# Optimization experiments

Hardware: AMD Instinct MI355X
Metric: run time of the kernel (lower is better)

The kernel has to match this reference:

```python
import jax, jax.numpy as jnp
import numpy as np

N, D, E, L, NL = 100000, 64, 400000, 4, 10000
NEG = jnp.float32(-1e30)


def _make_graph(key):
    k1, k2, k3, k4 = jax.random.split(key, 4)
    ncov = N - NL
    # nodes [0, NL) never appear as source -> exactly NL leaves
    src_cov = jnp.arange(ncov, dtype=jnp.int32) + NL
    src_rand = jax.random.randint(k1, (E - ncov,), NL, N, dtype=jnp.int32)
    src = jnp.concatenate([src_cov, src_rand])
    dst = jax.random.randint(k2, (E,), 0, N, dtype=jnp.int32)
    edge_index = jnp.stack([src, dst])  # [2, E]
    edge_attr = jax.random.normal(k3, (E, D), jnp.float32)
    # partition edges into L 'topological level' masks
    edge_masks = (jnp.arange(E) % L)[None, :] == jnp.arange(L)[:, None]  # [L, E] bool
    x = jax.random.normal(k4, (N, D), jnp.float32)
    return x, edge_index, edge_attr, edge_masks


def setup_inputs() -> dict:
    key = jax.random.key(0)
    kg1, kg2, kp = jax.random.split(key, 3)
    x1, ei1, ea1, em1 = _make_graph(kg1)
    x2, ei2, ea2, em2 = _make_graph(kg2)
    ks = jax.random.split(kp, 10)
    s = 1.0 / np.sqrt(D)
    params = {
        'We': jax.random.normal(ks[0], (D, D), jnp.float32) * s,
        'be': jax.random.normal(ks[1], (D,), jnp.float32) * s,
        'Wa': jax.random.normal(ks[2], (1, 2 * D), jnp.float32) * s,
        'ba': jax.random.normal(ks[3], (1,), jnp.float32) * s,
        'Wih': jax.random.normal(ks[4], (3 * D, D), jnp.float32) * s,
        'Whh': jax.random.normal(ks[5], (3 * D, D), jnp.float32) * s,
        'bih': jax.random.normal(ks[6], (3 * D,), jnp.float32) * s,
        'bhh': jax.random.normal(ks[7], (3 * D,), jnp.float32) * s,
        'Wc': jax.random.normal(ks[8], (2 * D, 2 * D), jnp.float32) * s,
        'bc': jax.random.normal(ks[9], (2 * D,), jnp.float32) * s,
    }
    return dict(x1=x1, edge_index1=ei1, edge_attr1=ea1, edge_masks1=em1,
                x2=x2, edge_index2=ei2, edge_attr2=ea2, edge_masks2=em2,
                **params, n_leaf=NL)


def _gru(x, h, Wih, Whh, bih, bhh):
    # torch.nn.GRUCell math
    gi = x @ Wih.T + bih
    gh = h @ Whh.T + bhh
    ir, iz, in_ = jnp.split(gi, 3, axis=-1)
    hr, hz, hn = jnp.split(gh, 3, axis=-1)
    r = jax.nn.sigmoid(ir + hr)
    z = jax.nn.sigmoid(iz + hz)
    n = jnp.tanh(in_ + r * hn)
    return (1.0 - z) * n + z * h


def _flow_forward(x, edge_index, edge_attr, edge_masks,
                  We, be, Wa, ba, Wih, Whh, bih, bhh):
    Nn, Dm = x.shape
    src, dst = edge_index[0], edge_index[1]
    root = jnp.ones((Nn,), bool).at[dst].set(False)  # nodes with no incoming edge
    eemb = edge_attr @ We.T + be                     # [E, D] edge_lin
    # roots: GRU with zero hidden; others start at 0 (zeros_like in torch)
    h0 = jnp.where(root[:, None], _gru(x, jnp.zeros_like(x), Wih, Whh, bih, bhh), 0.0)
    q = x[dst]                                       # h_prev_i, level-invariant

    def step(h, mask):
        k = h[src] + eemb                            # h_j + edge_emb
        logit = (jnp.concatenate([q, k], axis=-1) @ Wa.T + ba)[:, 0]  # [E]
        ml = jnp.where(mask, logit, NEG)
        mx = jnp.maximum(jax.ops.segment_max(ml, dst, num_segments=Nn), NEG)
        ex = jnp.where(mask, jnp.exp(ml - mx[dst]), 0.0)  # scatter-softmax numerator
        den = jax.ops.segment_sum(ex, dst, num_segments=Nn)
        alpha = ex / (den[dst] + 1e-16)
        msg = jax.ops.segment_sum(alpha[:, None] * h[src], dst, num_segments=Nn)
        nm = jax.ops.segment_sum(mask.astype(jnp.float32), dst, num_segments=Nn) > 0
        h_new = _gru(x, msg, Wih, Whh, bih, bhh)     # input=h_prev, hidden=msg
        return jnp.where(nm[:, None], h_new, h), None

    h, _ = jax.lax.scan(step, h0, edge_masks)
    return h


def reference(x1, edge_index1, edge_attr1, edge_masks1,
              x2, edge_index2, edge_attr2, edge_masks2,
              We, be, Wa, ba, Wih, Whh, bih, bhh, Wc, bc, n_leaf):
    o1 = _flow_forward(x1, edge_index1, edge_attr1, edge_masks1,
                       We, be, Wa, ba, Wih, Whh, bih, bhh)
    o2 = _flow_forward(x2, edge_index2, edge_attr2, edge_masks2,
                       We, be, Wa, ba, Wih, Whh, bih, bhh)
    Dm = x1.shape[1]
    leaf1 = jnp.ones((x1.shape[0],), bool).at[edge_index1[0]].set(False)
    leaf2 = jnp.ones((x2.shape[0],), bool).at[edge_index2[0]].set(False)
    idx1 = jnp.nonzero(leaf1, size=n_leaf)[0]
    idx2 = jnp.nonzero(leaf2, size=n_leaf)[0]
    feat = jnp.concatenate([o1[idx1], o2[idx2]], axis=-1) @ Wc.T + bc  # [NL, 2D]
    o1 = o1.at[idx1].set(feat[:, :Dm])
    o2 = o2.at[idx2].set(feat[:, Dm:])
    return (o1, o2)
```

## Files before the change

kernel.cpp:

```cpp
#include <hip/hip_runtime.h>

#define NN 100000
#define DD 64
#define EE 400000
#define LL 4
#define NLEAF 10000
#define NT (2*NN)
#define ETOT (2*EE)
#define M4 (4*NT)
#define NBLK ((M4 + 1023)/1024)

typedef __attribute__((ext_vector_type(8))) short bf8v;
typedef __attribute__((ext_vector_type(4))) float f4v;

__device__ __forceinline__ float rcp_(float x){ return __builtin_amdgcn_rcpf(x); }
__device__ __forceinline__ float sigm_(float x){ return rcp_(1.f + __expf(-x)); }
__device__ __forceinline__ float tanh_(float x){
  x = fminf(fmaxf(x, -15.f), 15.f);
  float a = __expf(2.f*x);
  return (a - 1.f) * rcp_(a + 1.f);
}
__device__ __forceinline__ float wave_sum(float p){
  #pragma unroll
  for (int m = 1; m < 64; m <<= 1) p += __shfl_xor(p, m, 64);
  return p;
}
__device__ __forceinline__ unsigned short f2b(float f){
  union { float f; unsigned int u; } v; v.f = f;
  unsigned int r = v.u + 0x7FFF + ((v.u >> 16) & 1);
  return (unsigned short)(r >> 16);
}
__device__ __forceinline__ float b2f(unsigned short b){
  union { unsigned int u; float f; } v; v.u = ((unsigned int)b) << 16;
  return v.f;
}

__global__ void k_init(int* __restrict__ counts, int* __restrict__ rootflag,
                       int* __restrict__ wlcnt, int* __restrict__ row_ptr,
                       float* __restrict__ hdot,
                       float* __restrict__ vvec, float* __restrict__ c0v,
                       unsigned short* __restrict__ whh_bf,
                       const float* __restrict__ We, const float* __restrict__ Wa,
                       const float* __restrict__ be, const float* __restrict__ Whh) {
  int tid = blockIdx.x*blockDim.x + threadIdx.x;
  int stride = gridDim.x*blockDim.x;
  for (int i = tid; i < M4; i += stride) counts[i] = 0;
  for (int i = tid; i < NT; i += stride) { rootflag[i] = 1; hdot[i] = 0.f; }
  for (int i = tid; i < 192*64; i += stride) whh_bf[i] = f2b(Whh[i]);
  if (blockIdx.x == 0 && threadIdx.x < 64) {
    int c = threadIdx.x;
    float acc = 0.f;
    for (int d = 0; d < 64; ++d) acc += We[d*64 + c] * Wa[64 + d];
    vvec[c] = acc;
    float p = wave_sum(be[c] * Wa[64 + c]);
    if (c == 0) { c0v[0] = p; row_ptr[M4] = ETOT; }
    if (c < 8) wlcnt[c] = 0;
  }
}

__global__ void k_edot(const float* __restrict__ ea1, const float* __restrict__ ea2,
                       const float* __restrict__ vvec, const float* __restrict__ c0v,
                       float* __restrict__ edot) {
  int lane = threadIdx.x & 63;
  int wave = blockIdx.x*(blockDim.x>>6) + (threadIdx.x>>6);
  int nw = gridDim.x*(blockDim.x>>6);
  int grp = lane >> 4, l16 = lane & 15;
  float4 v4 = ((const float4*)vvec)[l16];
  float c0 = c0v[0];
  for (int it = wave; it < ETOT/4; it += nw) {
    int ee = it*4 + grp;
    int g = ee >= EE;
    int e = ee - g*EE;
    const float* ea = g ? ea2 : ea1;
    float4 a = ((const float4*)(ea + (long)e*64))[l16];
    float p = a.x*v4.x + a.y*v4.y + a.z*v4.z + a.w*v4.w;
    p += __shfl_xor(p, 1, 64); p += __shfl_xor(p, 2, 64);
    p += __shfl_xor(p, 4, 64); p += __shfl_xor(p, 8, 64);
    if (l16 == 0) edot[ee] = p + c0;
  }
}

__global__ void k_count(const int* __restrict__ ei1, const int* __restrict__ ei2,
                        int* __restrict__ counts, int* __restrict__ rootflag) {
  int tid = blockIdx.x*blockDim.x + threadIdx.x;
  int stride = gridDim.x*blockDim.x;
  for (int ee = tid; ee < ETOT; ee += stride) {
    int g = ee >= EE;
    int e = ee - g*EE;
    const int* ei = g ? ei2 : ei1;
    int d = ei[EE + e];
    int l = e & 3;
    int td = g*NN + d;
    atomicAdd(&counts[l*NT + td], 1);
    rootflag[td] = 0;
  }
}

__global__ __launch_bounds__(256) void k_scan1(const int* __restrict__ counts,
                                               int* __restrict__ row_ptr,
                                               int* __restrict__ partials) {
  __shared__ int ts[256];
  int tx = threadIdx.x;
  int base = blockIdx.x*1024 + tx*4;
  int v[4]; int s = 0;
  #pragma unroll
  for (int u = 0; u < 4; ++u) { v[u] = (base+u < M4) ? counts[base+u] : 0; s += v[u]; }
  ts[tx] = s; __syncthreads();
  for (int off = 1; off < 256; off <<= 1) {
    int t = (tx >= off) ? ts[tx-off] : 0;
    __syncthreads();
    ts[tx] += t;
    __syncthreads();
  }
  int excl = ts[tx] - s;
  #pragma unroll
  for (int u = 0; u < 4; ++u) {
    if (base+u < M4) row_ptr[base+u] = excl;
    excl += v[u];
  }
  if (tx == 255) partials[blockIdx.x] = ts[255];
}

__global__ __launch_bounds__(256) void k_scan2(int* __restrict__ partials) {
  __shared__ int ts[256];
  int tx = threadIdx.x;
  int carry = 0;
  for (int base = 0; base < NBLK; base += 256) {
    int i = base + tx;
    int v = (i < NBLK) ? partials[i] : 0;
    ts[tx] = v; __syncthreads();
    for (int off = 1; off < 256; off <<= 1) {
      int t = (tx >= off) ? ts[tx-off] : 0;
      __syncthreads();
      ts[tx] += t;
      __syncthreads();
    }
    int incl = ts[tx];
    int tot = ts[255];
    __syncthreads();
    if (i < NBLK) partials[i] = incl - v + carry;
    carry += tot;
  }
}

__global__ __launch_bounds__(256) void k_scan3(int* __restrict__ row_ptr,
                                               const int* __restrict__ partials,
                                               const int* __restrict__ counts,
                                               int* __restrict__ wl, int* __restrict__ wlcnt) {
  __shared__ int cnt4[4];
  __shared__ int base4[4];
  int tx = threadIdx.x;
  if (tx < 4) cnt4[tx] = 0;
  __syncthreads();
  int base = blockIdx.x*1024 + tx*4;
  int add = partials[blockIdx.x];
  int rank[4]; int lvl[4]; bool val[4];
  #pragma unroll
  for (int u = 0; u < 4; ++u) {
    int i = base + u;
    val[u] = false;
    if (i < M4) {
      row_ptr[i] += add;
      if (counts[i] > 0) {
        int l = i / NT;
        lvl[u] = l;
        rank[u] = atomicAdd(&cnt4[l], 1);
        val[u] = true;
      }
    }
  }
  __syncthreads();
  if (tx < 4 && cnt4[tx] > 0) base4[tx] = atomicAdd(&wlcnt[tx], cnt4[tx]);
  __syncthreads();
  #pragma unroll
  for (int u = 0; u < 4; ++u) {
    if (val[u]) {
      int l = lvl[u];
      wl[l*NT + base4[l] + rank[u]] = (base + u) - l*NT;
    }
  }
}

__global__ void k_fill(const int* __restrict__ ei1, const int* __restrict__ ei2,
                       const float* __restrict__ edot, const float* __restrict__ ba,
                       const int* __restrict__ row_ptr, int* __restrict__ counts,
                       int* __restrict__ csr_src, float* __restrict__ csr_c) {
  int tid = blockIdx.x*blockDim.x + threadIdx.x;
  int stride = gridDim.x*blockDim.x;
  float bav = ba[0];
  for (int ee = tid; ee < ETOT; ee += stride) {
    int g = ee >= EE;
    int e = ee - g*EE;
    const int* ei = g ? ei2 : ei1;
    int s = ei[e], d = ei[EE + e];
    int l = e & 3;
    int i = l*NT + g*NN + d;
    int slot = atomicSub(&counts[i], 1) - 1;
    int pos = row_ptr[i] + slot;
    csr_src[pos] = g*NN + s;
    csr_c[pos] = edot[ee] + bav;
  }
}

__global__ __launch_bounds__(256) void k_gix(
    const float* __restrict__ x1, const float* __restrict__ x2,
    const float* __restrict__ Wih, const float* __restrict__ bih,
    const float* __restrict__ bhh, const float* __restrict__ Wa,
    const int* __restrict__ rootflag,
    ushort2* __restrict__ gi01, unsigned short* __restrict__ gi2p,
    float* __restrict__ xdot, float* __restrict__ hdot,
    float* __restrict__ hout, unsigned short* __restrict__ hbf) {
  __shared__ __align__(16) unsigned short Wb[208*72];
  __shared__ __align__(16) unsigned short xs[64*72];
  for (int i = threadIdx.x; i < 208*64; i += 256) {
    int n = i >> 6, k = i & 63;
    unsigned short v;
    if (n < 192)      v = f2b(Wih[n*64 + k]);
    else if (n == 192) v = f2b(Wa[k]);
    else               v = 0;
    Wb[n*72 + k] = v;
  }
  int lane = threadIdx.x & 63, w = threadIdx.x >> 6;
  int l15 = lane & 15, quad = lane >> 4;
  float bi0[4],bi1[4],bi2[4],bh0[4],bh1[4],bh2[4],wk4[4];
  #pragma unroll
  for (int tt = 0; tt < 4; ++tt) {
    int f = l15 + 16*tt;
    bi0[tt]=bih[f]; bi1[tt]=bih[64+f]; bi2[tt]=bih[128+f];
    bh0[tt]=bhh[f]; bh1[tt]=bhh[64+f]; bh2[tt]=bhh[128+f];
    wk4[tt]=Wa[64+f];
  }
  for (int ch = blockIdx.x; ch < NT/64; ch += gridDim.x) {
    int base = ch*64;
    __syncthreads();
    for (int i = threadIdx.x; i < 1024; i += 256) {
      int row = i >> 4, c4 = (i & 15)*4;
      int t = base + row;
      const float* xp = (t < NN) ? (x1 + (size_t)t*64) : (x2 + (size_t)(t-NN)*64);
      float4 v = ((const float4*)xp)[i & 15];
      ushort4 o; o.x=f2b(v.x); o.y=f2b(v.y); o.z=f2b(v.z); o.w=f2b(v.w);
      *(ushort4*)&xs[row*72 + c4] = o;
    }
    __syncthreads();
    bf8v a0 = *(const bf8v*)&xs[(w*16 + l15)*72 + quad*8];
    bf8v a1 = *(const bf8v*)&xs[(w*16 + l15)*72 + 32 + quad*8];
    f4v acc[13];
    #pragma unroll
    for (int nt = 0; nt < 13; ++nt) {
      bf8v b0 = *(const bf8v*)&Wb[(nt*16 + l15)*72 + quad*8];
      bf8v b1 = *(const bf8v*)&Wb[(nt*16 + l15)*72 + 32 + quad*8];
      f4v z = {0.f, 0.f, 0.f, 0.f};
      z = __builtin_amdgcn_mfma_f32_16x16x32_bf16(a0, b0, z, 0, 0, 0);
      acc[nt] = __builtin_amdgcn_mfma_f32_16x16x32_bf16(a1, b1, z, 0, 0, 0);
    }
    #pragma unroll
    for (int r = 0; r < 4; ++r) {
      int t = base + w*16 + quad*4 + r;
      int rt = rootflag[t];
      float hds = 0.f;
      #pragma unroll
      for (int tt = 0; tt < 4; ++tt) {
        int f = l15 + 16*tt;
        float g0 = acc[tt][r]   + bi0[tt];
        float g1 = acc[tt+4][r] + bi1[tt];
        float g2 = acc[tt+8][r] + bi2[tt];
        ushort2 p; p.x = f2b(g0); p.y = f2b(g1);
        gi01[(size_t)t*64 + f] = p;
        gi2p[(size_t)t*64 + f] = f2b(g2);
        float hv = 0.f;
        if (rt) {
          float rr = sigm_(g0 + bh0[tt]);
          float zz = sigm_(g1 + bh1[tt]);
          float nn = tanh_(g2 + rr*bh2[tt]);
          hv = (1.f - zz)*nn;
        }
        hout[(size_t)t*64 + f] = hv;
        hbf[(size_t)t*64 + f] = f2b(hv);
        hds += hv * wk4[tt];
      }
      if (rt) atomicAdd(&hdot[t], hds);
      if (l15 == 0) xdot[t] = acc[12][r];
    }
  }
}

__global__ void k_msg(const int* __restrict__ row_ptr, const int* __restrict__ csr_src,
                      const float* __restrict__ csr_c, const float* __restrict__ xdot,
                      const float* __restrict__ hdot, const unsigned short* __restrict__ hbf,
                      const int* __restrict__ wl, const int* __restrict__ wlcnt,
                      int level, unsigned short* __restrict__ msgn_bf) {
  int l16 = threadIdx.x & 15;
  int grp = (blockIdx.x*blockDim.x + threadIdx.x) >> 4;
  int ngrp = (gridDim.x*blockDim.x) >> 4;
  int cnt = wlcnt[level];
  for (int i = grp; i < cnt; i += ngrp) {
    int t = wl[level*NT + i];
    int bi = level*NT + t;
    int p0 = row_ptr[bi], p1 = row_ptr[bi+1];
    float xd = xdot[t];
    float den = 0.f;
    float m0 = 0.f, m1 = 0.f, m2 = 0.f, m3 = 0.f;
    for (int p = p0; p < p1; ++p) {
      int s = csr_src[p];
      float wv = __expf(xd + hdot[s] + csr_c[p]);
      den += wv;
      ushort4 hv = *(const ushort4*)(hbf + (size_t)s*64 + l16*4);
      m0 += wv*b2f(hv.x); m1 += wv*b2f(hv.y); m2 += wv*b2f(hv.z); m3 += wv*b2f(hv.w);
    }
    float rd = rcp_(den + 1e-16f);
    ushort4 o;
    o.x = f2b(m0*rd); o.y = f2b(m1*rd); o.z = f2b(m2*rd); o.w = f2b(m3*rd);
    *(ushort4*)(msgn_bf + (long)i*64 + l16*4) = o;
  }
}

__global__ __launch_bounds__(256) void k_gru(
    const unsigned short* __restrict__ whh_bf, const float* __restrict__ bhh,
    const float* __restrict__ Wa,
    const ushort2* __restrict__ gi01, const unsigned short* __restrict__ gi2p,
    const int* __restrict__ wl, const int* __restrict__ wlcnt, int level,
    const unsigned short* __restrict__ msgn_bf,
    float* __restrict__ hout, unsigned short* __restrict__ hbf,
    float* __restrict__ hdot) {
  int lane = threadIdx.x & 63, w = threadIdx.x >> 6;
  int l15 = lane & 15, quad = lane >> 4;
  int cnt = wlcnt[level];
  int ntile = (cnt + 15) >> 4;
  int wave = blockIdx.x*4 + w, nw = gridDim.x*4;
  float bh0[4], bh1[4], bh2[4], wk4[4];
  #pragma unroll
  for (int tt = 0; tt < 4; ++tt) {
    int f = tt*16 + l15;
    bh0[tt]=bhh[f]; bh1[tt]=bhh[64+f]; bh2[tt]=bhh[128+f];
    wk4[tt]=Wa[64+f];
  }
  for (int tl = wave; tl < ntile; tl += nw) {
    int base = tl*16;
    long abase = (long)(base + l15)*64;
    bf8v a0 = *(const bf8v*)&msgn_bf[abase + quad*8];
    bf8v a1 = *(const bf8v*)&msgn_bf[abase + 32 + quad*8];
    f4v acc[12];
    #pragma unroll
    for (int nt = 0; nt < 12; ++nt) {
      bf8v b0 = *(const bf8v*)&whh_bf[(nt*16 + l15)*64 + quad*8];
      bf8v b1 = *(const bf8v*)&whh_bf[(nt*16 + l15)*64 + 32 + quad*8];
      f4v z = {0.f, 0.f, 0.f, 0.f};
      z = __builtin_amdgcn_mfma_f32_16x16x32_bf16(a0, b0, z, 0, 0, 0);
      acc[nt] = __builtin_amdgcn_mfma_f32_16x16x32_bf16(a1, b1, z, 0, 0, 0);
    }
    #pragma unroll
    for (int r = 0; r < 4; ++r) {
      int i = base + quad*4 + r;
      if (i < cnt) {
        int t = wl[level*NT + i];
        float hds = 0.f;
        #pragma unroll
        for (int tt = 0; tt < 4; ++tt) {
          int f = tt*16 + l15;
          ushort2 p01 = gi01[(size_t)t*64 + f];
          float g2v = b2f(gi2p[(size_t)t*64 + f]);
          float mv  = b2f(msgn_bf[(long)i*64 + f]);
          float rr = sigm_(b2f(p01.x) + acc[tt][r]   + bh0[tt]);
          float zz = sigm_(b2f(p01.y) + acc[tt+4][r] + bh1[tt]);
          float nn = tanh_(g2v + rr*(acc[tt+8][r] + bh2[tt]));
          float hv = (1.f - zz)*nn + zz*mv;
          hout[(size_t)t*64 + f] = hv;
          hbf[(size_t)t*64 + f] = f2b(hv);
          hds += hv * wk4[tt];
        }
        hds += __shfl_xor(hds, 1, 64);
        hds += __shfl_xor(hds, 2, 64);
        hds += __shfl_xor(hds, 4, 64);
        hds += __shfl_xor(hds, 8, 64);
        if (l15 == 0) hdot[t] = hds;
      }
    }
  }
}

__global__ __launch_bounds__(256) void k_final(const float* __restrict__ Wc,
                                               const float* __restrict__ bc,
                                               float* __restrict__ hout) {
  __shared__ float WT[128*128];
  for (int idx = threadIdx.x; idx < 128*128; idx += 256) {
    int j = idx >> 7, c = idx & 127;
    WT[c*128 + j] = Wc[idx];
  }
  __syncthreads();
  int lane = threadIdx.x & 63, w = threadIdx.x >> 6;
  int wave = blockIdx.x*4 + w, nw = gridDim.x*4;
  float bc0 = bc[lane], bc1 = bc[64 + lane];
  for (int i = wave; i < NLEAF; i += nw) {
    float h1v = hout[(long)i*64 + lane];
    float h2v = hout[(long)(NN + i)*64 + lane];
    float acc0 = 0.f, acc1 = 0.f;
    for (int c = 0; c < 64; ++c) {
      float m1 = __shfl(h1v, c, 64);
      float m2 = __shfl(h2v, c, 64);
      acc0 += WT[c*128 + lane]      * m1 + WT[(64+c)*128 + lane]      * m2;
      acc1 += WT[c*128 + 64 + lane] * m1 + WT[(64+c)*128 + 64 + lane] * m2;
    }
    hout[(long)i*64 + lane]        = acc0 + bc0;
    hout[(long)(NN + i)*64 + lane] = acc1 + bc1;
  }
}

extern "C" void kernel_launch(void* const* d_in, const int* in_sizes, int n_in,
                              void* d_out, int out_size, void* d_ws, size_t ws_size,
                              hipStream_t stream) {
  const float* x1  = (const float*)d_in[0];
  const int*   ei1 = (const int*)  d_in[1];
  const float* ea1 = (const float*)d_in[2];
  const float* x2  = (const float*)d_in[4];
  const int*   ei2 = (const int*)  d_in[5];
  const float* ea2 = (const float*)d_in[6];
  const float* We  = (const float*)d_in[8];
  const float* be  = (const float*)d_in[9];
  const float* Wa  = (const float*)d_in[10];
  const float* ba  = (const float*)d_in[11];
  const float* Wih = (const float*)d_in[12];
  const float* Whh = (const float*)d_in[13];
  const float* bih = (const float*)d_in[14];
  const float* bhh = (const float*)d_in[15];
  const float* Wc  = (const float*)d_in[16];
  const float* bc  = (const float*)d_in[17];
  float* hout = (float*)d_out;

  float* f = (float*)d_ws;
  ushort2* gi01 = (ushort2*)f;        f += (size_t)NT*64;
  unsigned short* gi2p    = (unsigned short*)f;  f += (size_t)NT*32;
  unsigned short* msgn_bf = (unsigned short*)f;  f += (size_t)NT*32;
  unsigned short* hbf     = (unsigned short*)f;  f += (size_t)NT*32;
  unsigned short* whh_bf  = (unsigned short*)f;  f += 8192;
  float* edot = f;  f += ETOT;
  float* csr_c= f;  f += ETOT;
  float* xdot = f;  f += NT;
  float* hdot = f;  f += NT;
  float* vvec = f;  f += 64;
  float* c0v  = f;  f += 64;
  int* csr_src  = (int*)f;  f += ETOT;
  int* counts   = (int*)f;  f += M4;
  int* row_ptr  = (int*)f;  f += (M4 + 64);
  int* rootflag = (int*)f;  f += NT;
  int* wl       = (int*)f;  f += 4*NT;
  int* wlcnt    = (int*)f;  f += 64;
  int* partials = (int*)f;  f += 1024;

  k_init <<<dim3(512),  dim3(256), 0, stream>>>(counts, rootflag, wlcnt, row_ptr, hdot, vvec, c0v, whh_bf, We, Wa, be, Whh);
  k_edot <<<dim3(2048), dim3(256), 0, stream>>>(ea1, ea2, vvec, c0v, edot);
  k_count<<<dim3(512),  dim3(256), 0, stream>>>(ei1, ei2, counts, rootflag);
  k_scan1<<<dim3(NBLK), dim3(256), 0, stream>>>(counts, row_ptr, partials);
  k_scan2<<<dim3(1),    dim3(256), 0, stream>>>(partials);
  k_scan3<<<dim3(NBLK), dim3(256), 0, stream>>>(row_ptr, partials, counts, wl, wlcnt);
  k_fill <<<dim3(512),  dim3(256), 0, stream>>>(ei1, ei2, edot, ba, row_ptr, counts, csr_src, csr_c);
  k_gix  <<<dim3(1024), dim3(256), 0, stream>>>(x1, x2, Wih, bih, bhh, Wa, rootflag, gi01, gi2p, xdot, hdot, hout, hbf);
  for (int l = 0; l < 4; ++l) {
    k_msg<<<dim3(8192), dim3(256), 0, stream>>>(row_ptr, csr_src, csr_c, xdot, hdot, hbf, wl, wlcnt, l, msgn_bf);
    k_gru<<<dim3(2048), dim3(256), 0, stream>>>(whh_bf, bhh, Wa, gi01, gi2p, wl, wlcnt, l, msgn_bf, hout, hbf, hdot);
  }
  k_final<<<dim3(640), dim3(256), 0, stream>>>(Wc, bc, hout);
}
```

Measured before the change: 574.8 us.

## Interleave CSR arrays, pre-convert Wih once, and skip redundant h writes

```diff
diff --git a/kernel.cpp b/kernel.cpp
--- a/kernel.cpp
+++ b/kernel.cpp
@@ -40,13 +40,27 @@
                        float* __restrict__ hdot,
                        float* __restrict__ vvec, float* __restrict__ c0v,
                        unsigned short* __restrict__ whh_bf,
+                       unsigned short* __restrict__ wih_bf,
+                       unsigned short* __restrict__ hbf, int* __restrict__ lastlvl,
                        const float* __restrict__ We, const float* __restrict__ Wa,
-                       const float* __restrict__ be, const float* __restrict__ Whh) {
+                       const float* __restrict__ be, const float* __restrict__ Whh,
+                       const float* __restrict__ Wih) {
   int tid = blockIdx.x*blockDim.x + threadIdx.x;
   int stride = gridDim.x*blockDim.x;
   for (int i = tid; i < M4; i += stride) counts[i] = 0;
-  for (int i = tid; i < NT; i += stride) { rootflag[i] = 1; hdot[i] = 0.f; }
+  for (int i = tid; i < NT; i += stride) { rootflag[i] = 1; hdot[i] = 0.f; lastlvl[i] = -1; }
   for (int i = tid; i < 192*64; i += stride) whh_bf[i] = f2b(Whh[i]);
+  for (int i = tid; i < 208*64; i += stride) {
+    int n = i >> 6, k = i & 63;
+    unsigned short v;
+    if (n < 192)       v = f2b(Wih[i]);
+    else if (n == 192) v = f2b(Wa[k]);
+    else               v = 0;
+    wih_bf[i] = v;
+  }
+  uint4 z4 = make_uint4(0,0,0,0);
+  uint4* hz = (uint4*)hbf;
+  for (int i = tid; i < NT*8; i += stride) hz[i] = z4;
   if (blockIdx.x == 0 && threadIdx.x < 64) {
     int c = threadIdx.x;
     float acc = 0.f;
@@ -146,7 +160,8 @@
 __global__ __launch_bounds__(256) void k_scan3(int* __restrict__ row_ptr,
                                                const int* __restrict__ partials,
                                                const int* __restrict__ counts,
-                                               int* __restrict__ wl, int* __restrict__ wlcnt) {
+                                               int* __restrict__ wl, int* __restrict__ wlcnt,
+                                               int* __restrict__ lastlvl) {
   __shared__ int cnt4[4];
   __shared__ int base4[4];
   int tx = threadIdx.x;
@@ -166,6 +181,7 @@
         lvl[u] = l;
         rank[u] = atomicAdd(&cnt4[l], 1);
         val[u] = true;
+        atomicMax(&lastlvl[i - l*NT], l);
       }
     }
   }
@@ -184,7 +200,7 @@
 __global__ void k_fill(const int* __restrict__ ei1, const int* __restrict__ ei2,
                        const float* __restrict__ edot, const float* __restrict__ ba,
                        const int* __restrict__ row_ptr, int* __restrict__ counts,
-                       int* __restrict__ csr_src, float* __restrict__ csr_c) {
+                       int2* __restrict__ csr) {
   int tid = blockIdx.x*blockDim.x + threadIdx.x;
   int stride = gridDim.x*blockDim.x;
   float bav = ba[0];
@@ -197,31 +213,21 @@
     int i = l*NT + g*NN + d;
     int slot = atomicSub(&counts[i], 1) - 1;
     int pos = row_ptr[i] + slot;
-    csr_src[pos] = g*NN + s;
-    csr_c[pos] = edot[ee] + bav;
+    csr[pos] = make_int2(g*NN + s, __float_as_int(edot[ee] + bav));
   }
 }
 
 __global__ __launch_bounds__(256) void k_gix(
     const float* __restrict__ x1, const float* __restrict__ x2,
-    const float* __restrict__ Wih, const float* __restrict__ bih,
-    const float* __restrict__ bhh, const float* __restrict__ Wa,
-    const int* __restrict__ rootflag,
+    const unsigned short* __restrict__ wih_bf,
+    const float* __restrict__ bih, const float* __restrict__ bhh,
+    const float* __restrict__ Wa, const int* __restrict__ rootflag,
     ushort2* __restrict__ gi01, unsigned short* __restrict__ gi2p,
     float* __restrict__ xdot, float* __restrict__ hdot,
     float* __restrict__ hout, unsigned short* __restrict__ hbf) {
-  __shared__ __align__(16) unsigned short Wb[208*72];
-  __shared__ __align__(16) unsigned short xs[64*72];
-  for (int i = threadIdx.x; i < 208*64; i += 256) {
-    int n = i >> 6, k = i & 63;
-    unsigned short v;
-    if (n < 192)      v = f2b(Wih[n*64 + k]);
-    else if (n == 192) v = f2b(Wa[k]);
-    else               v = 0;
-    Wb[n*72 + k] = v;
-  }
   int lane = threadIdx.x & 63, w = threadIdx.x >> 6;
   int l15 = lane & 15, quad = lane >> 4;
+  int wave = blockIdx.x*4 + w, nw = gridDim.x*4;
   float bi0[4],bi1[4],bi2[4],bh0[4],bh1[4],bh2[4],wk4[4];
   #pragma unroll
   for (int tt = 0; tt < 4; ++tt) {
@@ -230,62 +236,79 @@
     bh0[tt]=bhh[f]; bh1[tt]=bhh[64+f]; bh2[tt]=bhh[128+f];
     wk4[tt]=Wa[64+f];
   }
-  for (int ch = blockIdx.x; ch < NT/64; ch += gridDim.x) {
-    int base = ch*64;
-    __syncthreads();
-    for (int i = threadIdx.x; i < 1024; i += 256) {
-      int row = i >> 4, c4 = (i & 15)*4;
-      int t = base + row;
-      const float* xp = (t < NN) ? (x1 + (size_t)t*64) : (x2 + (size_t)(t-NN)*64);
-      float4 v = ((const float4*)xp)[i & 15];
-      ushort4 o; o.x=f2b(v.x); o.y=f2b(v.y); o.z=f2b(v.z); o.w=f2b(v.w);
-      *(ushort4*)&xs[row*72 + c4] = o;
-    }
-    __syncthreads();
-    bf8v a0 = *(const bf8v*)&xs[(w*16 + l15)*72 + quad*8];
-    bf8v a1 = *(const bf8v*)&xs[(w*16 + l15)*72 + 32 + quad*8];
-    f4v acc[13];
+  for (int tl = wave; tl < NT/16; tl += nw) {
+    int ta = tl*16 + l15;
+    const float* xp = (ta < NN) ? x1 + (size_t)ta*64 : x2 + (size_t)(ta-NN)*64;
+    float4 v0 = ((const float4*)xp)[quad*2];
+    float4 v1 = ((const float4*)xp)[quad*2 + 1];
+    float4 v2 = ((const float4*)xp)[quad*2 + 8];
+    float4 v3 = ((const float4*)xp)[quad*2 + 9];
+    bf8v a0, a1;
+    a0[0]=(short)f2b(v0.x); a0[1]=(short)f2b(v0.y); a0[2]=(short)f2b(v0.z); a0[3]=(short)f2b(v0.w);
+    a0[4]=(short)f2b(v1.x); a0[5]=(short)f2b(v1.y); a0[6]=(short)f2b(v1.z); a0[7]=(short)f2b(v1.w);
+    a1[0]=(short)f2b(v2.x); a1[1]=(short)f2b(v2.y); a1[2]=(short)f2b(v2.z); a1[3]=(short)f2b(v2.w);
+    a1[4]=(short)f2b(v3.x); a1[5]=(short)f2b(v3.y); a1[6]=(short)f2b(v3.z); a1[7]=(short)f2b(v3.w);
+    int rt[4];
     #pragma unroll
-    for (int nt = 0; nt < 13; ++nt) {
-      bf8v b0 = *(const bf8v*)&Wb[(nt*16 + l15)*72 + quad*8];
-      bf8v b1 = *(const bf8v*)&Wb[(nt*16 + l15)*72 + 32 + quad*8];
-      f4v z = {0.f, 0.f, 0.f, 0.f};
-      z = __builtin_amdgcn_mfma_f32_16x16x32_bf16(a0, b0, z, 0, 0, 0);
-      acc[nt] = __builtin_amdgcn_mfma_f32_16x16x32_bf16(a1, b1, z, 0, 0, 0);
-    }
+    for (int r = 0; r < 4; ++r) rt[r] = rootflag[tl*16 + quad*4 + r];
+    float hds[4] = {0.f, 0.f, 0.f, 0.f};
     #pragma unroll
-    for (int r = 0; r < 4; ++r) {
-      int t = base + w*16 + quad*4 + r;
-      int rt = rootflag[t];
-      float hds = 0.f;
+    for (int tt = 0; tt < 4; ++tt) {
+      bf8v bR0 = *(const bf8v*)&wih_bf[((tt  )*16 + l15)*64 + quad*8];
+      bf8v bR1 = *(const bf8v*)&wih_bf[((tt  )*16 + l15)*64 + 32 + quad*8];
+      bf8v bZ0 = *(const bf8v*)&wih_bf[((tt+4)*16 + l15)*64 + quad*8];
+      bf8v bZ1 = *(const bf8v*)&wih_bf[((tt+4)*16 + l15)*64 + 32 + quad*8];
+      bf8v bN0 = *(const bf8v*)&wih_bf[((tt+8)*16 + l15)*64 + quad*8];
+      bf8v bN1 = *(const bf8v*)&wih_bf[((tt+8)*16 + l15)*64 + 32 + quad*8];
+      f4v zR = {0.f,0.f,0.f,0.f}, zZ = {0.f,0.f,0.f,0.f}, zN = {0.f,0.f,0.f,0.f};
+      zR = __builtin_amdgcn_mfma_f32_16x16x32_bf16(a0, bR0, zR, 0, 0, 0);
+      zR = __builtin_amdgcn_mfma_f32_16x16x32_bf16(a1, bR1, zR, 0, 0, 0);
+      zZ = __builtin_amdgcn_mfma_f32_16x16x32_bf16(a0, bZ0, zZ, 0, 0, 0);
+      zZ = __builtin_amdgcn_mfma_f32_16x16x32_bf16(a1, bZ1, zZ, 0, 0, 0);
+      zN = __builtin_amdgcn_mfma_f32_16x16x32_bf16(a0, bN0, zN, 0, 0, 0);
+      zN = __builtin_amdgcn_mfma_f32_16x16x32_bf16(a1, bN1, zN, 0, 0, 0);
+      int f = tt*16 + l15;
       #pragma unroll
-      for (int tt = 0; tt < 4; ++tt) {
-        int f = l15 + 16*tt;
-        float g0 = acc[tt][r]   + bi0[tt];
-        float g1 = acc[tt+4][r] + bi1[tt];
-        float g2 = acc[tt+8][r] + bi2[tt];
+      for (int r = 0; r < 4; ++r) {
+        int t = tl*16 + quad*4 + r;
+        float g0 = zR[r] + bi0[tt];
+        float g1 = zZ[r] + bi1[tt];
+        float g2 = zN[r] + bi2[tt];
         ushort2 p; p.x = f2b(g0); p.y = f2b(g1);
         gi01[(size_t)t*64 + f] = p;
         gi2p[(size_t)t*64 + f] = f2b(g2);
-        float hv = 0.f;
-        if (rt) {
+        if (rt[r]) {
           float rr = sigm_(g0 + bh0[tt]);
           float zz = sigm_(g1 + bh1[tt]);
           float nn = tanh_(g2 + rr*bh2[tt]);
-          hv = (1.f - zz)*nn;
+          float hv = (1.f - zz)*nn;
+          hout[(size_t)t*64 + f] = hv;
+          hbf[(size_t)t*64 + f] = f2b(hv);
+          hds[r] += hv * wk4[tt];
         }
-        hout[(size_t)t*64 + f] = hv;
-        hbf[(size_t)t*64 + f] = f2b(hv);
-        hds += hv * wk4[tt];
       }
-      if (rt) atomicAdd(&hdot[t], hds);
-      if (l15 == 0) xdot[t] = acc[12][r];
-    }
-  }
-}
-
-__global__ void k_msg(const int* __restrict__ row_ptr, const int* __restrict__ csr_src,
-                      const float* __restrict__ csr_c, const float* __restrict__ xdot,
+    }
+    bf8v bx0 = *(const bf8v*)&wih_bf[(192 + l15)*64 + quad*8];
+    bf8v bx1 = *(const bf8v*)&wih_bf[(192 + l15)*64 + 32 + quad*8];
+    f4v zX = {0.f,0.f,0.f,0.f};
+    zX = __builtin_amdgcn_mfma_f32_16x16x32_bf16(a0, bx0, zX, 0, 0, 0);
+    zX = __builtin_amdgcn_mfma_f32_16x16x32_bf16(a1, bx1, zX, 0, 0, 0);
+    #pragma unroll
+    for (int r = 0; r < 4; ++r) {
+      int t = tl*16 + quad*4 + r;
+      if (l15 == 0) xdot[t] = zX[r];
+      if (rt[r]) {
+        float h = hds[r];
+        h += __shfl_xor(h, 1, 64); h += __shfl_xor(h, 2, 64);
+        h += __shfl_xor(h, 4, 64); h += __shfl_xor(h, 8, 64);
+        if (l15 == 0) hdot[t] = h;
+      }
+    }
+  }
+}
+
+__global__ void k_msg(const int* __restrict__ row_ptr, const int2* __restrict__ csr,
+                      const float* __restrict__ xdot,
                       const float* __restrict__ hdot, const unsigned short* __restrict__ hbf,
                       const int* __restrict__ wl, const int* __restrict__ wlcnt,
                       int level, unsigned short* __restrict__ msgn_bf) {
@@ -301,8 +324,9 @@
     float den = 0.f;
     float m0 = 0.f, m1 = 0.f, m2 = 0.f, m3 = 0.f;
     for (int p = p0; p < p1; ++p) {
-      int s = csr_src[p];
-      float wv = __expf(xd + hdot[s] + csr_c[p]);
+      int2 pr = csr[p];
+      int s = pr.x;
+      float wv = __expf(xd + hdot[s] + __int_as_float(pr.y));
       den += wv;
       ushort4 hv = *(const ushort4*)(hbf + (size_t)s*64 + l16*4);
       m0 += wv*b2f(hv.x); m1 += wv*b2f(hv.y); m2 += wv*b2f(hv.z); m3 += wv*b2f(hv.w);
@@ -318,7 +342,8 @@
     const unsigned short* __restrict__ whh_bf, const float* __restrict__ bhh,
     const float* __restrict__ Wa,
     const ushort2* __restrict__ gi01, const unsigned short* __restrict__ gi2p,
-    const int* __restrict__ wl, const int* __restrict__ wlcnt, int level,
+    const int* __restrict__ wl, const int* __restrict__ wlcnt,
+    const int* __restrict__ lastlvl, int level,
     const unsigned short* __restrict__ msgn_bf,
     float* __restrict__ hout, unsigned short* __restrict__ hbf,
     float* __restrict__ hdot) {
@@ -353,6 +378,7 @@
       int i = base + quad*4 + r;
       if (i < cnt) {
         int t = wl[level*NT + i];
+        int ll = lastlvl[t];
         float hds = 0.f;
         #pragma unroll
         for (int tt = 0; tt < 4; ++tt) {
@@ -364,15 +390,17 @@
           float zz = sigm_(b2f(p01.y) + acc[tt+4][r] + bh1[tt]);
           float nn = tanh_(g2v + rr*(acc[tt+8][r] + bh2[tt]));
           float hv = (1.f - zz)*nn + zz*mv;
-          hout[(size_t)t*64 + f] = hv;
-          hbf[(size_t)t*64 + f] = f2b(hv);
+          if (ll == level) hout[(size_t)t*64 + f] = hv;
+          if (level < 3)  hbf[(size_t)t*64 + f] = f2b(hv);
           hds += hv * wk4[tt];
         }
-        hds += __shfl_xor(hds, 1, 64);
-        hds += __shfl_xor(hds, 2, 64);
-        hds += __shfl_xor(hds, 4, 64);
-        hds += __shfl_xor(hds, 8, 64);
-        if (l15 == 0) hdot[t] = hds;
+        if (level < 3) {
+          hds += __shfl_xor(hds, 1, 64);
+          hds += __shfl_xor(hds, 2, 64);
+          hds += __shfl_xor(hds, 4, 64);
+          hds += __shfl_xor(hds, 8, 64);
+          if (l15 == 0) hdot[t] = hds;
+        }
       }
     }
   }
@@ -432,31 +460,32 @@
   unsigned short* msgn_bf = (unsigned short*)f;  f += (size_t)NT*32;
   unsigned short* hbf     = (unsigned short*)f;  f += (size_t)NT*32;
   unsigned short* whh_bf  = (unsigned short*)f;  f += 8192;
+  unsigned short* wih_bf  = (unsigned short*)f;  f += 8192;
   float* edot = f;  f += ETOT;
-  float* csr_c= f;  f += ETOT;
   float* xdot = f;  f += NT;
   float* hdot = f;  f += NT;
   float* vvec = f;  f += 64;
   float* c0v  = f;  f += 64;
-  int* csr_src  = (int*)f;  f += ETOT;
+  int2* csr     = (int2*)f; f += (size_t)2*ETOT;
   int* counts   = (int*)f;  f += M4;
   int* row_ptr  = (int*)f;  f += (M4 + 64);
   int* rootflag = (int*)f;  f += NT;
+  int* lastlvl  = (int*)f;  f += NT;
   int* wl       = (int*)f;  f += 4*NT;
   int* wlcnt    = (int*)f;  f += 64;
   int* partials = (int*)f;  f += 1024;
 
-  k_init <<<dim3(512),  dim3(256), 0, stream>>>(counts, rootflag, wlcnt, row_ptr, hdot, vvec, c0v, whh_bf, We, Wa, be, Whh);
+  k_init <<<dim3(1024), dim3(256), 0, stream>>>(counts, rootflag, wlcnt, row_ptr, hdot, vvec, c0v, whh_bf, wih_bf, hbf, lastlvl, We, Wa, be, Whh, Wih);
   k_edot <<<dim3(2048), dim3(256), 0, stream>>>(ea1, ea2, vvec, c0v, edot);
   k_count<<<dim3(512),  dim3(256), 0, stream>>>(ei1, ei2, counts, rootflag);
   k_scan1<<<dim3(NBLK), dim3(256), 0, stream>>>(counts, row_ptr, partials);
   k_scan2<<<dim3(1),    dim3(256), 0, stream>>>(partials);
-  k_scan3<<<dim3(NBLK), dim3(256), 0, stream>>>(row_ptr, partials, counts, wl, wlcnt);
-  k_fill <<<dim3(512),  dim3(256), 0, stream>>>(ei1, ei2, edot, ba, row_ptr, counts, csr_src, csr_c);
-  k_gix  <<<dim3(1024), dim3(256), 0, stream>>>(x1, x2, Wih, bih, bhh, Wa, rootflag, gi01, gi2p, xdot, hdot, hout, hbf);
+  k_scan3<<<dim3(NBLK), dim3(256), 0, stream>>>(row_ptr, partials, counts, wl, wlcnt, lastlvl);
+  k_fill <<<dim3(512),  dim3(256), 0, stream>>>(ei1, ei2, edot, ba, row_ptr, counts, csr);
+  k_gix  <<<dim3(2048), dim3(256), 0, stream>>>(x1, x2, wih_bf, bih, bhh, Wa, rootflag, gi01, gi2p, xdot, hdot, hout, hbf);
   for (int l = 0; l < 4; ++l) {
-    k_msg<<<dim3(8192), dim3(256), 0, stream>>>(row_ptr, csr_src, csr_c, xdot, hdot, hbf, wl, wlcnt, l, msgn_bf);
-    k_gru<<<dim3(2048), dim3(256), 0, stream>>>(whh_bf, bhh, Wa, gi01, gi2p, wl, wlcnt, l, msgn_bf, hout, hbf, hdot);
+    k_msg<<<dim3(8192), dim3(256), 0, stream>>>(row_ptr, csr, xdot, hdot, hbf, wl, wlcnt, l, msgn_bf);
+    k_gru<<<dim3(2048), dim3(256), 0, stream>>>(whh_bf, bhh, Wa, gi01, gi2p, wl, wlcnt, lastlvl, l, msgn_bf, hout, hbf, hdot);
   }
   k_final<<<dim3(640), dim3(256), 0, stream>>>(Wc, bc, hout);
 }
```

After: 583.5 us. No clear change (+1.5%).
